# Optimization experiments

Hardware: AMD Instinct MI355X
Metric: run time of the kernel (lower is better)

The kernel has to match this reference:

```python
import jax, jax.numpy as jnp
import numpy as np

C = 64


def setup_inputs() -> dict:
    key = jax.random.key(0)
    ks = jax.random.split(key, 7)
    x = jax.random.normal(ks[0], (8, C, 64, 64), dtype=jnp.float32)
    # 1x1 conv weights stored as [out_c, in_c]; biases [out_c]
    s = 1.0 / np.sqrt(C)
    W1 = jax.random.uniform(ks[1], (C, C), jnp.float32, -s, s)
    b1 = jax.random.uniform(ks[2], (C,), jnp.float32, -s, s)
    W2 = jax.random.uniform(ks[3], (C, C), jnp.float32, -s, s)
    b2 = jax.random.uniform(ks[4], (C,), jnp.float32, -s, s)
    W3 = jax.random.uniform(ks[5], (C, C), jnp.float32, -s, s)
    b3 = jax.random.uniform(ks[6], (C,), jnp.float32, -s, s)
    return {"x": x, "W1": W1, "b1": b1, "W2": W2, "b2": b2, "W3": W3, "b3": b3}


def reference(x, W1, b1, W2, b2, W3, b3):
    gamma = 1.0
    b, c, h, w = x.shape
    xf = x.reshape(b, c, h * w)  # [b, c, n]
    # 1x1 convs == per-pixel channel matmuls
    f = jnp.einsum('oc,bcn->bon', W1, xf) + b1[None, :, None]
    g = jnp.einsum('oc,bcn->bon', W2, xf) + b2[None, :, None]
    k = jnp.einsum('oc,bcn->bon', W3, xf) + b3[None, :, None]
    # scores[b,i,j] = sum_c f[b,c,i] * g[b,c,j]; softmax over j
    scores = jnp.einsum('bci,bcj->bij', f, g)
    attn = jax.nn.softmax(scores, axis=2)
    # out_attn[b,c,i] = sum_j attn[b,i,j] * k[b,c,j]
    out = jnp.einsum('bij,bcj->bci', attn, k).reshape(b, c, h, w)
    return gamma * out + x
```

## Files before the change

kernel.cpp:

```cpp
#include <hip/hip_runtime.h>
#include <hip/hip_bf16.h>

#define NPIX 4096
#define CCH  64
#define NB   8
#define KVBLK 64

typedef __attribute__((ext_vector_type(8)))  short short8;
typedef __attribute__((ext_vector_type(4)))  float f32x4;
typedef __attribute__((ext_vector_type(16))) float f32x16;

#define LOG2E   1.44269504f

__global__ __launch_bounds__(256) void proj_kernel(
    const float* __restrict__ x,
    const float* __restrict__ W1, const float* __restrict__ b1,
    const float* __restrict__ W2, const float* __restrict__ b2,
    const float* __restrict__ W3, const float* __restrict__ b3,
    __hip_bfloat16* __restrict__ Q, __hip_bfloat16* __restrict__ G,
    __hip_bfloat16* __restrict__ K)
{
    const int b  = blockIdx.x >> 6;
    const int i0 = (blockIdx.x & 63) << 6;

    __shared__ float xs[64][65];
    __shared__ float Wt[3][64][68];

    for (int e = threadIdx.x; e < 4096; e += 256) {
        const int c = e >> 6, p = e & 63;
        xs[c][p] = x[(size_t)b * CCH * NPIX + (size_t)c * NPIX + i0 + p];
        Wt[0][e & 63][e >> 6] = W1[e];
        Wt[1][e & 63][e >> 6] = W2[e];
        Wt[2][e & 63][e >> 6] = W3[e];
    }
    __syncthreads();

    const int p = threadIdx.x & 63;
    const int g = threadIdx.x >> 6;

    float acc0[16], acc1[16], acc2[16];
    #pragma unroll
    for (int oo = 0; oo < 16; ++oo) {
        acc0[oo] = b1[g * 16 + oo];
        acc1[oo] = b2[g * 16 + oo];
        acc2[oo] = b3[g * 16 + oo];
    }

    for (int c = 0; c < 64; ++c) {
        const float xv = xs[c][p];
        const f32x4* w0 = (const f32x4*)&Wt[0][c][g * 16];
        const f32x4* w1 = (const f32x4*)&Wt[1][c][g * 16];
        const f32x4* w2 = (const f32x4*)&Wt[2][c][g * 16];
        #pragma unroll
        for (int q = 0; q < 4; ++q) {
            const f32x4 a = w0[q], bb = w1[q], cc = w2[q];
            #pragma unroll
            for (int j = 0; j < 4; ++j) {
                acc0[q * 4 + j] += a[j] * xv;
                acc1[q * 4 + j] += bb[j] * xv;
                acc2[q * 4 + j] += cc[j] * xv;
            }
        }
    }

    const int i = i0 + p;
    #pragma unroll
    for (int oo = 0; oo < 16; ++oo) {
        const int oc = g * 16 + oo;
        Q[(size_t)b * NPIX * CCH + (size_t)i * CCH + oc] = __float2bfloat16(acc0[oo] * LOG2E);
        G[(size_t)b * NPIX * CCH + (size_t)i * CCH + oc] = __float2bfloat16(acc1[oo]);
        K[(size_t)b * CCH * NPIX + (size_t)oc * NPIX + i] = __float2bfloat16(acc2[oo]);
    }
}

__device__ __forceinline__ void gload_lds16(const void* g, void* l) {
    __builtin_amdgcn_global_load_lds(
        (const __attribute__((address_space(1))) unsigned int*)g,
        (__attribute__((address_space(3))) unsigned int*)l, 16, 0, 0);
}
__device__ __forceinline__ unsigned int cvtpk_bf16(float lo, float hi) {
    unsigned int r;
    asm("v_cvt_pk_bf16_f32 %0, %1, %2" : "=v"(r) : "v"(lo), "v"(hi));
    return r;
}
__device__ __forceinline__ float exp2_raw(float x) {
    float r;
    asm("v_exp_f32 %0, %1\n\ts_nop 1" : "=v"(r) : "v"(x));
    return r;
}

__global__ __launch_bounds__(512, 4) void attn_kernel(
    const __hip_bfloat16* __restrict__ Qg, const __hip_bfloat16* __restrict__ Gg,
    const __hip_bfloat16* __restrict__ Kg,
    __hip_bfloat16* __restrict__ Opart, float* __restrict__ Lpart, int split)
{
    __shared__ char lds[2][16384];

    const int blk   = blockIdx.x;
    const int per_b = 16 * split;
    const int b     = blk / per_b;
    const int rem   = blk - b * per_b;
    const int itile = rem / split;
    const int sp    = rem - itile * split;
    const int tid   = threadIdx.x;
    const int wave  = tid >> 6;
    const int lane  = tid & 63;
    const int l32   = lane & 31;
    const int hi    = lane >> 5;
    const int i0w   = itile * 256 + wave * 32;
    const int jcnt  = NPIX / split;
    const int jlo   = sp * jcnt;
    const int niter = jcnt / KVBLK;

    const short* Qb = (const short*)Qg + (size_t)b * NPIX * CCH;
    const char*  Gb = (const char*)(Gg + (size_t)b * NPIX * CCH);
    const char*  Kb = (const char*)(Kg + (size_t)b * CCH * NPIX);

    short8 q[4];
    #pragma unroll
    for (int ks = 0; ks < 4; ++ks)
        q[ks] = *(const short8*)(Qb + (size_t)(i0w + l32) * CCH + ks * 16 + hi * 8);

    int gbase[2], kbase[2];
    #pragma unroll
    for (int jb = 0; jb < 2; ++jb)
        gbase[jb] = (jb * 32 + l32) * 128 + ((l32 & 7) << 4);
    #pragma unroll
    for (int cb = 0; cb < 2; ++cb)
        kbase[cb] = 8192 + (cb * 32 + l32) * 128 + ((l32 & 7) << 4);

    const int srow = tid >> 3, scolb = (tid & 7) * 16;
    const char* gsrc = Gb + (size_t)(jlo + srow) * 128 + (scolb ^ ((srow & 7) << 4));
    const char* ksrc = Kb + (size_t)srow * 8192 + (size_t)jlo * 2 + (scolb ^ ((srow & 7) << 4));

    f32x16 zacc;
    #pragma unroll
    for (int r = 0; r < 16; ++r) zacc[r] = 0.f;

    f32x16 o[2];
    #pragma unroll
    for (int cb = 0; cb < 2; ++cb)
        #pragma unroll
        for (int r = 0; r < 16; ++r) o[cb][r] = 0.f;
    float ps = 0.f;

    auto STAGE = [&](int buf, int tt) {
        gload_lds16(gsrc + tt * (KVBLK * 128), lds[buf] + wave * 1024);
        gload_lds16(ksrc + tt * (KVBLK * 2),  lds[buf] + 8192 + wave * 1024);
    };

    STAGE(0, 0);
    __syncthreads();

    for (int t = 0; t < niter; ++t) {
        const int cur = t & 1;
        STAGE(cur ^ 1, (t + 1 < niter) ? t + 1 : 0);
        const char* L = lds[cur];

        #pragma unroll
        for (int jb = 0; jb < 2; ++jb) {
            short8 ga[4];
            #pragma unroll
            for (int ks = 0; ks < 4; ++ks)
                ga[ks] = *(const short8*)(L + (gbase[jb] ^ ((2 * ks + hi) << 4)));

            __builtin_amdgcn_s_setprio(1);
            f32x16 acc = __builtin_amdgcn_mfma_f32_32x32x16_bf16(ga[0], q[0], zacc, 0, 0, 0);
            acc = __builtin_amdgcn_mfma_f32_32x32x16_bf16(ga[1], q[1], acc, 0, 0, 0);
            acc = __builtin_amdgcn_mfma_f32_32x32x16_bf16(ga[2], q[2], acc, 0, 0, 0);
            acc = __builtin_amdgcn_mfma_f32_32x32x16_bf16(ga[3], q[3], acc, 0, 0, 0);
            __builtin_amdgcn_s_setprio(0);

            float p[16];
            #pragma unroll
            for (int r = 0; r < 16; ++r) {
                const float a = __builtin_amdgcn_fmed3f(acc[r], acc[r], acc[r]);
                p[r] = exp2_raw(a);
                ps += p[r];
            }
            short8 pf[2];
            #pragma unroll
            for (int kk = 0; kk < 2; ++kk) {
                unsigned int x0 = cvtpk_bf16(p[8 * kk + 0], p[8 * kk + 1]);
                unsigned int x1 = cvtpk_bf16(p[8 * kk + 2], p[8 * kk + 3]);
                unsigned int y0 = cvtpk_bf16(p[8 * kk + 4], p[8 * kk + 5]);
                unsigned int y1 = cvtpk_bf16(p[8 * kk + 6], p[8 * kk + 7]);
                asm("v_permlane32_swap_b32 %0, %1" : "+v"(x0), "+v"(y0));
                asm("v_permlane32_swap_b32 %0, %1" : "+v"(x1), "+v"(y1));
                union { unsigned int u[4]; short8 v; } w;
                w.u[0] = x0; w.u[1] = x1; w.u[2] = y0; w.u[3] = y1;
                pf[kk] = w.v;
            }

            __builtin_amdgcn_s_setprio(1);
            #pragma unroll
            for (int kk = 0; kk < 2; ++kk) {
                const int ksg = 2 * jb + kk;
                const short8 ka0 = *(const short8*)(L + (kbase[0] ^ ((2 * ksg + hi) << 4)));
                const short8 ka1 = *(const short8*)(L + (kbase[1] ^ ((2 * ksg + hi) << 4)));
                o[0] = __builtin_amdgcn_mfma_f32_32x32x16_bf16(ka0, pf[kk], o[0], 0, 0, 0);
                o[1] = __builtin_amdgcn_mfma_f32_32x32x16_bf16(ka1, pf[kk], o[1], 0, 0, 0);
            }
            __builtin_amdgcn_s_setprio(0);
        }
        __syncthreads();
    }

    const size_t pb = (size_t)(b * split + sp);
    #pragma unroll
    for (int cb = 0; cb < 2; ++cb)
        #pragma unroll
        for (int r = 0; r < 16; ++r) {
            const int c = cb * 32 + (r & 3) + 8 * (r >> 2) + 4 * hi;
            const int i = i0w + l32;
            Opart[(pb * CCH + c) * NPIX + i] = __float2bfloat16(o[cb][r]);
        }
    ps += __shfl_xor(ps, 32);
    if (lane < 32)
        Lpart[pb * NPIX + i0w + l32] = ps;
}

__global__ __launch_bounds__(256) void combine_kernel(
    const __hip_bfloat16* __restrict__ Opart, const float* __restrict__ Lpart,
    const float* __restrict__ x, float* __restrict__ out, int split)
{
    const int b = blockIdx.x >> 6, c = blockIdx.x & 63;
    #pragma unroll
    for (int chunk = 0; chunk < 2; ++chunk) {
        const int i = chunk * 2048 + threadIdx.x * 8;
        float acc[8] = {0,0,0,0,0,0,0,0};
        float Ls[8]  = {0,0,0,0,0,0,0,0};
        for (int s = 0; s < split; ++s) {
            const size_t pb = (size_t)(b * split + s);
            const short8 ov = *(const short8*)((const short*)Opart + (pb * CCH + c) * NPIX + i);
            const f32x4 l0 = *(const f32x4*)&Lpart[pb * NPIX + i];
            const f32x4 l1 = *(const f32x4*)&Lpart[pb * NPIX + i + 4];
            #pragma unroll
            for (int t = 0; t < 8; ++t) {
                union { unsigned int u; float f; } cv;
                cv.u = ((unsigned int)(unsigned short)ov[t]) << 16;
                acc[t] += cv.f;
                Ls[t]  += (t < 4) ? l0[t] : l1[t - 4];
            }
        }
        const size_t idx = ((size_t)b * CCH + c) * NPIX + i;
        const f32x4 xv0 = *(const f32x4*)&x[idx];
        const f32x4 xv1 = *(const f32x4*)&x[idx + 4];
        f32x4 r0, r1;
        #pragma unroll
        for (int t = 0; t < 4; ++t) {
            r0[t] = acc[t] / Ls[t] + xv0[t];
            r1[t] = acc[t + 4] / Ls[t + 4] + xv1[t];
        }
        *(f32x4*)&out[idx]     = r0;
        *(f32x4*)&out[idx + 4] = r1;
    }
}

extern "C" void kernel_launch(void* const* d_in, const int* in_sizes, int n_in,
                              void* d_out, int out_size, void* d_ws, size_t ws_size,
                              hipStream_t stream) {
    const float* x  = (const float*)d_in[0];
    const float* W1 = (const float*)d_in[1];
    const float* b1 = (const float*)d_in[2];
    const float* W2 = (const float*)d_in[3];
    const float* b2 = (const float*)d_in[4];
    const float* W3 = (const float*)d_in[5];
    const float* b3 = (const float*)d_in[6];
    float* out = (float*)d_out;

    char* ws = (char*)d_ws;
    const size_t planeB = (size_t)NB * NPIX * CCH * sizeof(__hip_bfloat16);
    __hip_bfloat16* Q = (__hip_bfloat16*)(ws);
    __hip_bfloat16* G = (__hip_bfloat16*)(ws + planeB);
    __hip_bfloat16* K = (__hip_bfloat16*)(ws + 2 * planeB);

    const size_t base   = 3 * planeB;
    const size_t oPlane = planeB;
    const size_t lPlane = (size_t)NB * NPIX * sizeof(float);

    int split = 8;
    while (split > 1 && base + (size_t)split * (oPlane + lPlane) > ws_size)
        split >>= 1;

    __hip_bfloat16* Opart = (__hip_bfloat16*)(ws + base);
    float* Lpart = (float*)(ws + base + (size_t)split * oPlane);

    proj_kernel<<<dim3(NB * 64), dim3(256), 0, stream>>>(x, W1, b1, W2, b2, W3, b3, Q, G, K);
    attn_kernel<<<dim3(NB * 16 * split), dim3(512), 0, stream>>>(Q, G, K, Opart, Lpart, split);
    combine_kernel<<<dim3(NB * CCH), dim3(256), 0, stream>>>(Opart, Lpart, x, out, split);
}
```

Baseline: 86.56 us.

## Drop LDS staging in projection and replace inline asm with builtins in attention

The projection kernel no longer stages x and the transposed weights in shared memory. Each thread holds its 64 input channels in registers and reads weight rows directly from global memory, which are wave-uniform and likely become scalar loads. In the attention kernel, the inline-asm exp2 (with its fmed3 and nop) and bf16 pack are replaced by compiler builtins, letting the compiler schedule them. The risks are high register pressure in the projection and possibly slower generic bf16 conversion code.

```diff
diff --git a/kernel.cpp b/kernel.cpp
--- a/kernel.cpp
+++ b/kernel.cpp
@@ -22,54 +22,35 @@
 {
     const int b  = blockIdx.x >> 6;
     const int i0 = (blockIdx.x & 63) << 6;
-
-    __shared__ float xs[64][65];
-    __shared__ float Wt[3][64][68];
-
-    for (int e = threadIdx.x; e < 4096; e += 256) {
-        const int c = e >> 6, p = e & 63;
-        xs[c][p] = x[(size_t)b * CCH * NPIX + (size_t)c * NPIX + i0 + p];
-        Wt[0][e & 63][e >> 6] = W1[e];
-        Wt[1][e & 63][e >> 6] = W2[e];
-        Wt[2][e & 63][e >> 6] = W3[e];
-    }
-    __syncthreads();
-
-    const int p = threadIdx.x & 63;
-    const int g = threadIdx.x >> 6;
-
-    float acc0[16], acc1[16], acc2[16];
-    #pragma unroll
-    for (int oo = 0; oo < 16; ++oo) {
-        acc0[oo] = b1[g * 16 + oo];
-        acc1[oo] = b2[g * 16 + oo];
-        acc2[oo] = b3[g * 16 + oo];
-    }
-
-    for (int c = 0; c < 64; ++c) {
-        const float xv = xs[c][p];
-        const f32x4* w0 = (const f32x4*)&Wt[0][c][g * 16];
-        const f32x4* w1 = (const f32x4*)&Wt[1][c][g * 16];
-        const f32x4* w2 = (const f32x4*)&Wt[2][c][g * 16];
-        #pragma unroll
-        for (int q = 0; q < 4; ++q) {
-            const f32x4 a = w0[q], bb = w1[q], cc = w2[q];
-            #pragma unroll
-            for (int j = 0; j < 4; ++j) {
-                acc0[q * 4 + j] += a[j] * xv;
-                acc1[q * 4 + j] += bb[j] * xv;
-                acc2[q * 4 + j] += cc[j] * xv;
-            }
-        }
-    }
-
-    const int i = i0 + p;
-    #pragma unroll
-    for (int oo = 0; oo < 16; ++oo) {
-        const int oc = g * 16 + oo;
-        Q[(size_t)b * NPIX * CCH + (size_t)i * CCH + oc] = __float2bfloat16(acc0[oo] * LOG2E);
-        G[(size_t)b * NPIX * CCH + (size_t)i * CCH + oc] = __float2bfloat16(acc1[oo]);
-        K[(size_t)b * CCH * NPIX + (size_t)oc * NPIX + i] = __float2bfloat16(acc2[oo]);
+    const int p  = threadIdx.x & 63;
+    const int g  = threadIdx.x >> 6;
+    const int i  = i0 + p;
+
+    float xv[64];
+    #pragma unroll
+    for (int c = 0; c < 64; ++c)
+        xv[c] = x[(size_t)b * CCH * NPIX + (size_t)c * NPIX + i];
+
+    const float* Ws[3] = {W1, W2, W3};
+    const float* bs[3] = {b1, b2, b3};
+
+    #pragma unroll
+    for (int m = 0; m < 3; ++m) {
+        #pragma unroll
+        for (int oo = 0; oo < 16; ++oo) {
+            const int oc = g * 16 + oo;
+            const float* wrow = Ws[m] + oc * 64;
+            float a = bs[m][oc];
+            #pragma unroll
+            for (int c = 0; c < 64; ++c)
+                a += wrow[c] * xv[c];
+            if (m == 0)
+                Q[(size_t)b * NPIX * CCH + (size_t)i * CCH + oc] = __float2bfloat16(a * LOG2E);
+            else if (m == 1)
+                G[(size_t)b * NPIX * CCH + (size_t)i * CCH + oc] = __float2bfloat16(a);
+            else
+                K[(size_t)b * CCH * NPIX + (size_t)oc * NPIX + i] = __float2bfloat16(a);
+        }
     }
 }
 
@@ -78,15 +59,10 @@
         (const __attribute__((address_space(1))) unsigned int*)g,
         (__attribute__((address_space(3))) unsigned int*)l, 16, 0, 0);
 }
-__device__ __forceinline__ unsigned int cvtpk_bf16(float lo, float hi) {
-    unsigned int r;
-    asm("v_cvt_pk_bf16_f32 %0, %1, %2" : "=v"(r) : "v"(lo), "v"(hi));
-    return r;
-}
-__device__ __forceinline__ float exp2_raw(float x) {
-    float r;
-    asm("v_exp_f32 %0, %1\n\ts_nop 1" : "=v"(r) : "v"(x));
-    return r;
+__device__ __forceinline__ unsigned int pack_bf16(float lo, float hi) {
+    union { __hip_bfloat162 h; unsigned int u; } w;
+    w.h = __float22bfloat162_rn(make_float2(lo, hi));
+    return w.u;
 }
 
 __global__ __launch_bounds__(512, 4) void attn_kernel(
@@ -174,17 +150,16 @@
             float p[16];
             #pragma unroll
             for (int r = 0; r < 16; ++r) {
-                const float a = __builtin_amdgcn_fmed3f(acc[r], acc[r], acc[r]);
-                p[r] = exp2_raw(a);
+                p[r] = __builtin_amdgcn_exp2f(acc[r]);
                 ps += p[r];
             }
             short8 pf[2];
             #pragma unroll
             for (int kk = 0; kk < 2; ++kk) {
-                unsigned int x0 = cvtpk_bf16(p[8 * kk + 0], p[8 * kk + 1]);
-                unsigned int x1 = cvtpk_bf16(p[8 * kk + 2], p[8 * kk + 3]);
-                unsigned int y0 = cvtpk_bf16(p[8 * kk + 4], p[8 * kk + 5]);
-                unsigned int y1 = cvtpk_bf16(p[8 * kk + 6], p[8 * kk + 7]);
+                unsigned int x0 = pack_bf16(p[8 * kk + 0], p[8 * kk + 1]);
+                unsigned int x1 = pack_bf16(p[8 * kk + 2], p[8 * kk + 3]);
+                unsigned int y0 = pack_bf16(p[8 * kk + 4], p[8 * kk + 5]);
+                unsigned int y1 = pack_bf16(p[8 * kk + 6], p[8 * kk + 7]);
                 asm("v_permlane32_swap_b32 %0, %1" : "+v"(x0), "+v"(y0));
                 asm("v_permlane32_swap_b32 %0, %1" : "+v"(x1), "+v"(y1));
                 union { unsigned int u[4]; short8 v; } w;
```

Result: slower. 129.0 us (+49.0%).
